# Performance work log

Measured on AMD Instinct MI355X. Metric: run time of the kernel, lower is better.

The kernel has to match this reference:

```python
import jax, jax.numpy as jnp
import numpy as np
from jax import lax

D_MODEL = 2048
D_INNER = 4096  # expand * d_model
D_CONV = 4
B, T = 4, 2048


def _rmsnorm(h):
    # F.normalize(x, dim=-1) * sqrt(D): x / max(||x||_2, 1e-12) * sqrt(D)
    n = jnp.sqrt(jnp.sum(h * h, axis=-1, keepdims=True))
    return h / jnp.maximum(n, 1e-12) * (h.shape[-1] ** 0.5)


def setup_inputs() -> dict:
    key = jax.random.key(0)
    ks = jax.random.split(key, 7)
    std = 0.02
    return {
        "x": jax.random.normal(ks[0], (B, T, D_MODEL), jnp.float32),
        "W_in": jax.random.normal(ks[1], (2 * D_INNER, D_MODEL), jnp.float32) * std,
        "conv_w": jax.random.normal(ks[2], (D_INNER, 1, D_CONV), jnp.float32) * std,
        "conv_b": jnp.zeros((D_INNER,), jnp.float32),
        "W_out": jax.random.normal(ks[3], (D_MODEL, D_INNER), jnp.float32) * std,
        "W_mlp1": jax.random.normal(ks[4], (4 * D_MODEL, D_MODEL), jnp.float32) * std,
        "W_mlp2": jax.random.normal(ks[5], (D_MODEL, 4 * D_MODEL), jnp.float32) * std,
    }


def _mamba_fallback(h, W_in, conv_w, conv_b, W_out):
    # in_proj: (B,T,D) -> (B,T,2*d_inner), split into x branch and gate z
    xz = jnp.einsum("btd,ed->bte", h, W_in)
    xp, z = jnp.split(xz, 2, axis=-1)
    # depthwise causal conv over time: torch pads (d_conv-1) both sides then slices [:T]
    # == left-pad-only causal cross-correlation
    xc = lax.conv_general_dilated(
        xp.transpose(0, 2, 1),  # (B, d_inner, T)
        conv_w,                  # (d_inner, 1, d_conv)
        window_strides=(1,),
        padding=[(D_CONV - 1, 0)],
        dimension_numbers=("NCH", "OIH", "NCH"),
        feature_group_count=D_INNER,
    ) + conv_b[None, :, None]
    xc = xc.transpose(0, 2, 1)  # (B, T, d_inner)
    y = jax.nn.silu(xc) * jax.nn.silu(z)
    return jnp.einsum("bte,de->btd", y, W_out)


def reference(x, W_in, conv_w, conv_b, W_out, W_mlp1, W_mlp2):
    # full-dimension path (active_dim=None)
    h = _rmsnorm(x)
    x = x + _mamba_fallback(h, W_in, conv_w, conv_b, W_out)
    h = _rmsnorm(x)
    m = jnp.einsum("bte,de->btd", jax.nn.relu(jnp.einsum("btd,ed->bte", h, W_mlp1)), W_mlp2)
    return x + m
```

## Files before the change

### kernel.cpp

```cpp
#include <hip/hip_runtime.h>
#include <hip/hip_bf16.h>

typedef __bf16 bf16;
typedef __bf16 bf16x8 __attribute__((ext_vector_type(8)));
typedef float f32x4 __attribute__((ext_vector_type(4)));

#define D_MODEL 2048
#define D_INNER 4096
#define ROWS    8192

__device__ __forceinline__ void gload_lds16(const void* g, void* l) {
    __builtin_amdgcn_global_load_lds(
        (const __attribute__((address_space(1))) void*)g,
        (__attribute__((address_space(3))) void*)l, 16, 0, 0);
}

__global__ __launch_bounds__(256) void f2b_kernel(const float* __restrict__ in,
                                                  bf16* __restrict__ out, int n8) {
    int i = blockIdx.x * 256 + threadIdx.x;
    if (i >= n8) return;
    long base = (long)i * 8;
    float4 a = *(const float4*)(in + base);
    float4 b = *(const float4*)(in + base + 4);
    bf16x8 o;
    o[0] = (bf16)a.x; o[1] = (bf16)a.y; o[2] = (bf16)a.z; o[3] = (bf16)a.w;
    o[4] = (bf16)b.x; o[5] = (bf16)b.y; o[6] = (bf16)b.z; o[7] = (bf16)b.w;
    *(bf16x8*)(out + base) = o;
}

__global__ __launch_bounds__(256) void rmsnorm_kernel(const float* __restrict__ x,
                                                      bf16* __restrict__ h) {
    const long row = blockIdx.x;
    const float* xr = x + row * D_MODEL;
    float4 v0 = ((const float4*)xr)[threadIdx.x * 2];
    float4 v1 = ((const float4*)xr)[threadIdx.x * 2 + 1];
    float ss = v0.x*v0.x + v0.y*v0.y + v0.z*v0.z + v0.w*v0.w
             + v1.x*v1.x + v1.y*v1.y + v1.z*v1.z + v1.w*v1.w;
    #pragma unroll
    for (int o = 32; o; o >>= 1) ss += __shfl_xor(ss, o, 64);
    __shared__ float red[4];
    if ((threadIdx.x & 63) == 0) red[threadIdx.x >> 6] = ss;
    __syncthreads();
    float tot = red[0] + red[1] + red[2] + red[3];
    float scale = 45.254834f / fmaxf(sqrtf(tot), 1e-12f);
    bf16x8 o;
    o[0] = (bf16)(v0.x*scale); o[1] = (bf16)(v0.y*scale);
    o[2] = (bf16)(v0.z*scale); o[3] = (bf16)(v0.w*scale);
    o[4] = (bf16)(v1.x*scale); o[5] = (bf16)(v1.y*scale);
    o[6] = (bf16)(v1.z*scale); o[7] = (bf16)(v1.w*scale);
    *(bf16x8*)(h + row * D_MODEL + threadIdx.x * 8) = o;
}

__global__ __launch_bounds__(256) void conv_gate_kernel(bf16* __restrict__ xz,
                                                        const float* __restrict__ cw,
                                                        const float* __restrict__ cb) {
    const int idx = blockIdx.x * 256 + threadIdx.x;
    const int c8  = idx & 511;
    const int row = idx >> 9;
    const int t   = row & 2047;
    const int c0  = c8 * 8;
    float acc[8];
    float wv[8][4];
    #pragma unroll
    for (int e = 0; e < 8; ++e) {
        float4 f = ((const float4*)cw)[c0 + e];
        wv[e][0] = f.x; wv[e][1] = f.y; wv[e][2] = f.z; wv[e][3] = f.w;
        acc[e] = cb[c0 + e];
    }
    #pragma unroll
    for (int j = 0; j < 4; ++j) {
        if (t + j - 3 >= 0) {
            bf16x8 xv = *(const bf16x8*)(xz + (long)(row + j - 3) * (2*D_INNER) + c0);
            #pragma unroll
            for (int e = 0; e < 8; ++e) acc[e] += (float)xv[e] * wv[e][j];
        }
    }
    bf16* zp = xz + (long)row * (2*D_INNER) + D_INNER + c0;
    bf16x8 zv = *(const bf16x8*)zp;
    bf16x8 yv;
    #pragma unroll
    for (int e = 0; e < 8; ++e) {
        float xc = acc[e];
        float s1 = xc / (1.f + __expf(-xc));
        float z  = (float)zv[e];
        float s2 = z / (1.f + __expf(-z));
        yv[e] = (bf16)(s1 * s2);
    }
    *(bf16x8*)zp = yv;
}

template<int EPI>
__global__ __launch_bounds__(512, 2) void gemm_bt(
        const bf16* __restrict__ A, long lda,
        const bf16* __restrict__ B,
        void* __restrict__ C, const float* __restrict__ res,
        int N, int K, int gx) {
    __shared__ __align__(16) char LB[131072];
    const int tid = threadIdx.x;
    const int w   = tid >> 6;
    const int l   = tid & 63;
    const int lr  = l & 15;

    const int nwg = gridDim.x;
    const int qq  = nwg >> 3;
    const int sw  = (blockIdx.x & 7) * qq + (blockIdx.x >> 3);
    const int bx  = sw % gx, by = sw / gx;
    const long rowBase = (long)by * 256;
    const long colBase = (long)bx * 256;

    const int srow = w * 8 + (l >> 3);
    const int schk = (l & 7) ^ ((l >> 3) & 7);
    const bf16* aSrc = A + (rowBase + srow) * lda + schk * 8;
    const bf16* bSrc = B + (colBase + srow) * (long)K + schk * 8;
    const long lda64 = 64 * lda;
    const long ldb64 = 64 * (long)K;
    const int  w1024 = w * 1024;

    auto stgA = [&](int DBB, int kt) {
        const bf16* s = aSrc + (long)kt * 64;
        gload_lds16(s,            LB + DBB +     0 + w1024);
        gload_lds16(s +   lda64,  LB + DBB +  8192 + w1024);
        gload_lds16(s + 2*lda64,  LB + DBB + 16384 + w1024);
        gload_lds16(s + 3*lda64,  LB + DBB + 24576 + w1024);
    };
    auto stgB = [&](int DBB, int kt) {
        const bf16* s = bSrc + (long)kt * 64;
        gload_lds16(s,            LB + DBB + 32768 + w1024);
        gload_lds16(s +   ldb64,  LB + DBB + 40960 + w1024);
        gload_lds16(s + 2*ldb64,  LB + DBB + 49152 + w1024);
        gload_lds16(s + 3*ldb64,  LB + DBB + 57344 + w1024);
    };

    const int cx0 = (((l >> 4)    ) ^ (l & 7)) << 4;
    const int cx1 = (((l >> 4) + 4) ^ (l & 7)) << 4;
    const int hm = w >> 2;
    const int q  = w & 3;
    int aRow[8], bRow[4];
    #pragma unroll
    for (int m = 0; m < 8; ++m) aRow[m] = hm * 16384 + (m * 16 + lr) * 128;
    #pragma unroll
    for (int n = 0; n < 4; ++n)
        bRow[n] = 32768 + (q >> 1) * 16384 + ((q & 1) * 64 + n * 16 + lr) * 128;

    const int nt  = K >> 6;
    const int nit = nt >> 1;
    f32x4 acc[8][4] = {};
    bf16x8 AX[4][2], BL[2][2], BH[2][2];

    stgB(0, 0);      stgA(0, 0);
    stgB(65536, 1);  stgA(65536, 1);
    asm volatile("s_waitcnt vmcnt(8)" ::: "memory");
    __builtin_amdgcn_s_barrier();
    __builtin_amdgcn_sched_barrier(0);
    #pragma unroll
    for (int m = 0; m < 4; ++m) {
        AX[m][0] = *(const bf16x8*)(LB + aRow[m] + cx0);
        AX[m][1] = *(const bf16x8*)(LB + aRow[m] + cx1);
    }
    #pragma unroll
    for (int n = 0; n < 2; ++n) {
        BL[n][0] = *(const bf16x8*)(LB + bRow[n]     + cx0);
        BL[n][1] = *(const bf16x8*)(LB + bRow[n]     + cx1);
        BH[n][0] = *(const bf16x8*)(LB + bRow[n + 2] + cx0);
        BH[n][1] = *(const bf16x8*)(LB + bRow[n + 2] + cx1);
    }
    asm volatile("s_waitcnt lgkmcnt(0)" ::: "memory");
    __builtin_amdgcn_sched_barrier(0);
    __builtin_amdgcn_s_setprio(1);
    #pragma unroll
    for (int m = 0; m < 4; ++m)
        #pragma unroll
        for (int n = 0; n < 2; ++n) {
            acc[m][n] = __builtin_amdgcn_mfma_f32_16x16x32_bf16(AX[m][0], BL[n][0], acc[m][n], 0, 0, 0);
            acc[m][n] = __builtin_amdgcn_mfma_f32_16x16x32_bf16(AX[m][1], BL[n][1], acc[m][n], 0, 0, 0);
        }
    __builtin_amdgcn_s_setprio(0);
    __builtin_amdgcn_s_barrier();

    for (int it = 0; it < nit; ++it) {
        int kA = 2 * it + 2; if (kA >= nt) kA = 0;
        int kB = 2 * it + 3; if (kB >= nt) kB = 0;
        #pragma unroll
        for (int db = 0; db < 2; ++db) {
            const int DBB = db * 65536;
            const char* Lb = LB + DBB;
            const char* Ln = LB + (DBB ^ 65536);
            const int kst = db ? kB : kA;
            const bool full = (db == 0) || (it < nit - 1);

            stgB(DBB, kst);
            __builtin_amdgcn_s_setprio(1);
            #pragma unroll
            for (int m = 0; m < 4; ++m)
                #pragma unroll
                for (int n = 0; n < 2; ++n) {
                    acc[m][n + 2] = __builtin_amdgcn_mfma_f32_16x16x32_bf16(AX[m][0], BH[n][0], acc[m][n + 2], 0, 0, 0);
                    acc[m][n + 2] = __builtin_amdgcn_mfma_f32_16x16x32_bf16(AX[m][1], BH[n][1], acc[m][n + 2], 0, 0, 0);
                }
            __builtin_amdgcn_s_setprio(0);
            asm volatile("s_waitcnt vmcnt(4)" ::: "memory");
            __builtin_amdgcn_sched_barrier(0);
            #pragma unroll
            for (int m = 0; m < 4; ++m) {
                AX[m][0] = *(const bf16x8*)(Lb + aRow[m + 4] + cx0);
                AX[m][1] = *(const bf16x8*)(Lb + aRow[m + 4] + cx1);
            }
            asm volatile("s_waitcnt lgkmcnt(0)" ::: "memory");
            __builtin_amdgcn_sched_barrier(0);
            __builtin_amdgcn_s_setprio(1);
            #pragma unroll
            for (int m = 0; m < 4; ++m)
                #pragma unroll
                for (int n = 0; n < 2; ++n) {
                    acc[m + 4][n + 2] = __builtin_amdgcn_mfma_f32_16x16x32_bf16(AX[m][0], BH[n][0], acc[m + 4][n + 2], 0, 0, 0);
                    acc[m + 4][n + 2] = __builtin_amdgcn_mfma_f32_16x16x32_bf16(AX[m][1], BH[n][1], acc[m + 4][n + 2], 0, 0, 0);
                }
            __builtin_amdgcn_s_setprio(0);
            __builtin_amdgcn_s_barrier();

            __builtin_amdgcn_s_setprio(1);
            #pragma unroll
            for (int m = 0; m < 4; ++m)
                #pragma unroll
                for (int n = 0; n < 2; ++n) {
                    acc[m + 4][n] = __builtin_amdgcn_mfma_f32_16x16x32_bf16(AX[m][0], BL[n][0], acc[m + 4][n], 0, 0, 0);
                    acc[m + 4][n] = __builtin_amdgcn_mfma_f32_16x16x32_bf16(AX[m][1], BL[n][1], acc[m + 4][n], 0, 0, 0);
                }
            __builtin_amdgcn_s_setprio(0);
            __builtin_amdgcn_sched_barrier(0);
            stgA(DBB, kst);
            if (full) {
                #pragma unroll
                for (int m = 0; m < 4; ++m) {
                    AX[m][0] = *(const bf16x8*)(Ln + aRow[m] + cx0);
                    AX[m][1] = *(const bf16x8*)(Ln + aRow[m] + cx1);
                }
                #pragma unroll
                for (int n = 0; n < 2; ++n) {
                    BL[n][0] = *(const bf16x8*)(Ln + bRow[n]     + cx0);
                    BL[n][1] = *(const bf16x8*)(Ln + bRow[n]     + cx1);
                    BH[n][0] = *(const bf16x8*)(Ln + bRow[n + 2] + cx0);
                    BH[n][1] = *(const bf16x8*)(Ln + bRow[n + 2] + cx1);
                }
                asm volatile("s_waitcnt lgkmcnt(0)" ::: "memory");
                __builtin_amdgcn_sched_barrier(0);
                __builtin_amdgcn_s_setprio(1);
                #pragma unroll
                for (int m = 0; m < 4; ++m)
                    #pragma unroll
                    for (int n = 0; n < 2; ++n) {
                        acc[m][n] = __builtin_amdgcn_mfma_f32_16x16x32_bf16(AX[m][0], BL[n][0], acc[m][n], 0, 0, 0);
                        acc[m][n] = __builtin_amdgcn_mfma_f32_16x16x32_bf16(AX[m][1], BL[n][1], acc[m][n], 0, 0, 0);
                    }
                __builtin_amdgcn_s_setprio(0);
            }
            __builtin_amdgcn_s_barrier();
        }
    }

    asm volatile("s_waitcnt vmcnt(0)" ::: "memory");

    const int lg = l >> 4;
    const long wrow = rowBase + hm * 128;
    const long wcol = colBase + q * 64;
    #pragma unroll
    for (int m = 0; m < 8; ++m) {
        #pragma unroll
        for (int n = 0; n < 4; ++n) {
            f32x4 v = acc[m][n];
            #pragma unroll
            for (int r = 0; r < 4; ++r) {
                long row = wrow + m*16 + lg*4 + r;
                long col = wcol + n*16 + lr;
                long off = row * N + col;
                if (EPI == 0)      ((bf16*)C)[off] = (bf16)v[r];
                else if (EPI == 1) ((bf16*)C)[off] = (bf16)fmaxf(v[r], 0.f);
                else               ((float*)C)[off] = res[off] + v[r];
            }
        }
    }
}

extern "C" void kernel_launch(void* const* d_in, const int* in_sizes, int n_in,
                              void* d_out, int out_size, void* d_ws, size_t ws_size,
                              hipStream_t stream) {
    const float* x      = (const float*)d_in[0];
    const float* W_in   = (const float*)d_in[1];
    const float* cw     = (const float*)d_in[2];
    const float* cb     = (const float*)d_in[3];
    const float* W_out  = (const float*)d_in[4];
    const float* W_mlp1 = (const float*)d_in[5];
    const float* W_mlp2 = (const float*)d_in[6];
    float* out = (float*)d_out;

    char* ws  = (char*)d_ws;
    bf16* wW  = (bf16*)(ws);
    bf16* h   = (bf16*)(ws + 33554432);
    bf16* xz  = (bf16*)(ws + 67108864);
    float* x2 = (float*)(ws + 201326592);
    bf16* y   = xz + D_INNER;
    bf16* m1  = xz;

    dim3 blk(256);
    dim3 gblk(512);

    f2b_kernel<<<dim3(8192), blk, 0, stream>>>(W_in, wW, 16777216/8);
    rmsnorm_kernel<<<dim3(ROWS), blk, 0, stream>>>(x, h);
    gemm_bt<0><<<dim3(1024), gblk, 0, stream>>>(h, D_MODEL, wW, xz, nullptr, 2*D_INNER, D_MODEL, 32);
    conv_gate_kernel<<<dim3(16384), blk, 0, stream>>>(xz, cw, cb);
    f2b_kernel<<<dim3(4096), blk, 0, stream>>>(W_out, wW, 8388608/8);
    gemm_bt<2><<<dim3(256), gblk, 0, stream>>>(y, 2*D_INNER, wW, x2, x, D_MODEL, D_INNER, 8);

    rmsnorm_kernel<<<dim3(ROWS), blk, 0, stream>>>(x2, h);
    f2b_kernel<<<dim3(8192), blk, 0, stream>>>(W_mlp1, wW, 16777216/8);
    gemm_bt<1><<<dim3(1024), gblk, 0, stream>>>(h, D_MODEL, wW, m1, nullptr, 4*D_MODEL, D_MODEL, 32);
    f2b_kernel<<<dim3(8192), blk, 0, stream>>>(W_mlp2, wW, 16777216/8);
    gemm_bt<2><<<dim3(256), gblk, 0, stream>>>(m1, 4*D_MODEL, wW, out, x2, D_MODEL, 4*D_MODEL, 8);
}
```

Before: 1.007 ms.

## Stage GEMM epilogue through swizzled LDS for vectorized coalesced stores; relax lgkmcnt wait

The GEMM epilogue now writes each wave's accumulator tile into a swizzled region of LDS and reads it back, so global stores become 16-byte coalesced row writes instead of scattered scalar bf16/fp32 stores. The residual-add path also reads the residual with float4 loads, and it processes the tile in two halves to fit within each wave's 16 KB slice. Separately, the fragment loads are split so the first MFMA batch waits only until the A and BL fragments have arrived (lgkmcnt(4)), overlapping the BH loads with compute. The change adds LDS traffic and a barrier before the epilogue, and it depends on the lgkmcnt count matching the compiler's actual ordering of the LDS loads.

```diff
diff --git a/kernel.cpp b/kernel.cpp
--- a/kernel.cpp
+++ b/kernel.cpp
@@ -161,10 +161,13 @@
     for (int n = 0; n < 2; ++n) {
         BL[n][0] = *(const bf16x8*)(LB + bRow[n]     + cx0);
         BL[n][1] = *(const bf16x8*)(LB + bRow[n]     + cx1);
+    }
+    #pragma unroll
+    for (int n = 0; n < 2; ++n) {
         BH[n][0] = *(const bf16x8*)(LB + bRow[n + 2] + cx0);
         BH[n][1] = *(const bf16x8*)(LB + bRow[n + 2] + cx1);
     }
-    asm volatile("s_waitcnt lgkmcnt(0)" ::: "memory");
+    asm volatile("s_waitcnt lgkmcnt(4)" ::: "memory");
     __builtin_amdgcn_sched_barrier(0);
     __builtin_amdgcn_s_setprio(1);
     #pragma unroll
@@ -239,10 +242,13 @@
                 for (int n = 0; n < 2; ++n) {
                     BL[n][0] = *(const bf16x8*)(Ln + bRow[n]     + cx0);
                     BL[n][1] = *(const bf16x8*)(Ln + bRow[n]     + cx1);
+                }
+                #pragma unroll
+                for (int n = 0; n < 2; ++n) {
                     BH[n][0] = *(const bf16x8*)(Ln + bRow[n + 2] + cx0);
                     BH[n][1] = *(const bf16x8*)(Ln + bRow[n + 2] + cx1);
                 }
-                asm volatile("s_waitcnt lgkmcnt(0)" ::: "memory");
+                asm volatile("s_waitcnt lgkmcnt(4)" ::: "memory");
                 __builtin_amdgcn_sched_barrier(0);
                 __builtin_amdgcn_s_setprio(1);
                 #pragma unroll
@@ -259,24 +265,62 @@
     }
 
     asm volatile("s_waitcnt vmcnt(0)" ::: "memory");
+    __builtin_amdgcn_s_barrier();
 
     const int lg = l >> 4;
     const long wrow = rowBase + hm * 128;
     const long wcol = colBase + q * 64;
-    #pragma unroll
-    for (int m = 0; m < 8; ++m) {
-        #pragma unroll
-        for (int n = 0; n < 4; ++n) {
-            f32x4 v = acc[m][n];
-            #pragma unroll
-            for (int r = 0; r < 4; ++r) {
-                long row = wrow + m*16 + lg*4 + r;
-                long col = wcol + n*16 + lr;
-                long off = row * N + col;
-                if (EPI == 0)      ((bf16*)C)[off] = (bf16)v[r];
-                else if (EPI == 1) ((bf16*)C)[off] = (bf16)fmaxf(v[r], 0.f);
-                else               ((float*)C)[off] = res[off] + v[r];
-            }
+    char* ep = LB + w * 16384;
+
+    if (EPI == 2) {
+        #pragma unroll
+        for (int mh = 0; mh < 2; ++mh) {
+            #pragma unroll
+            for (int m = 0; m < 4; ++m) {
+                #pragma unroll
+                for (int n = 0; n < 4; ++n) {
+                    f32x4 v = acc[mh * 4 + m][n];
+                    #pragma unroll
+                    for (int r = 0; r < 4; ++r) {
+                        int rowr = m * 16 + lg * 4 + r;
+                        int chnk = (n * 4 + (lr >> 2)) ^ (rowr & 7);
+                        *(float*)(ep + rowr * 256 + chnk * 16 + (lr & 3) * 4) = v[r];
+                    }
+                }
+            }
+            asm volatile("s_waitcnt lgkmcnt(0)" ::: "memory");
+            #pragma unroll
+            for (int i = 0; i < 16; ++i) {
+                int rr = i * 4 + (l >> 4);
+                float4 lv = *(float4*)(ep + rr * 256 + (((l & 15) ^ (rr & 7)) * 16));
+                long off = (wrow + mh * 64 + rr) * N + wcol + (l & 15) * 4;
+                float4 rv = *(const float4*)(res + off);
+                lv.x += rv.x; lv.y += rv.y; lv.z += rv.z; lv.w += rv.w;
+                *(float4*)((float*)C + off) = lv;
+            }
+            if (mh == 0) { asm volatile("s_waitcnt lgkmcnt(0) vmcnt(0)" ::: "memory"); }
+        }
+    } else {
+        #pragma unroll
+        for (int m = 0; m < 8; ++m) {
+            #pragma unroll
+            for (int n = 0; n < 4; ++n) {
+                f32x4 v = acc[m][n];
+                #pragma unroll
+                for (int r = 0; r < 4; ++r) {
+                    int rowr = m * 16 + lg * 4 + r;
+                    int chnk = (n * 2 + (lr >> 3)) ^ (rowr & 7);
+                    float val = (EPI == 1) ? fmaxf(v[r], 0.f) : v[r];
+                    *(bf16*)(ep + rowr * 128 + chnk * 16 + (lr & 7) * 2) = (bf16)val;
+                }
+            }
+        }
+        asm volatile("s_waitcnt lgkmcnt(0)" ::: "memory");
+        #pragma unroll
+        for (int i = 0; i < 16; ++i) {
+            int rr = i * 8 + (l >> 3);
+            uint4 lv = *(uint4*)(ep + rr * 128 + (((l & 7) ^ (rr & 7)) * 16));
+            *(uint4*)((bf16*)C + (wrow + rr) * N + wcol + (l & 7) * 8) = lv;
         }
     }
 }
```

New measurement: 1.003 ms. About the same (-0.4%).
